# Kernel tuning notes

Hardware: AMD Instinct MI355X
Metric: run time of the kernel (lower is better)

The kernel has to match this reference:

```python
import jax, jax.numpy as jnp
import numpy as np

N = 200000      # nodes (Elliptic-scale transaction graph)
E = 400000      # directed edges
F_IN = 165      # node features
HID = 128
OUT = 2


def setup_inputs() -> dict:
    key = jax.random.key(0)
    k = jax.random.split(key, 5)
    x = jax.random.normal(k[0], (N, F_IN), dtype=jnp.float32)
    edge_index = jax.random.randint(k[1], (2, E), 0, N, dtype=jnp.int32)
    # GCNConv params (PyG: Linear without bias semantics differ slightly by
    # version; here weight + bias, bias added after aggregation)
    W1 = jax.random.normal(k[2], (F_IN, HID), dtype=jnp.float32) * (1.0 / np.sqrt(F_IN))
    b1 = jnp.zeros((HID,), dtype=jnp.float32)
    W2 = jax.random.normal(k[3], (HID, OUT), dtype=jnp.float32) * (1.0 / np.sqrt(HID))
    b2 = jnp.zeros((OUT,), dtype=jnp.float32)
    return {"x": x, "edge_index": edge_index, "W1": W1, "b1": b1, "W2": W2, "b2": b2}


def _gcn_conv(h, edge_index, W, b):
    """PyG GCNConv: out = D^{-1/2} (A + I) D^{-1/2} (h @ W) + b."""
    h = h @ W                                    # [N, F_out]
    loop = jnp.arange(N, dtype=edge_index.dtype)
    src = jnp.concatenate([edge_index[0], loop])  # add self-loops
    dst = jnp.concatenate([edge_index[1], loop])
    # degree over destination nodes (self-loops guarantee deg >= 1)
    deg = jax.ops.segment_sum(jnp.ones_like(dst, dtype=h.dtype), dst, num_segments=N)
    dinv = jax.lax.rsqrt(deg)
    norm = dinv[src] * dinv[dst]                 # [E+N]
    msgs = h[src] * norm[:, None]                # gather + scale
    out = jax.ops.segment_sum(msgs, dst, num_segments=N)  # scatter-add
    return out + b


def reference(x, edge_index, W1, b1, W2, b2):
    h = _gcn_conv(x, edge_index, W1, b1)
    # torch.relu then F.dropout(training=False) (identity) then torch.relu:
    # in eval mode relu(relu(h)) == relu(h)
    h = jnp.maximum(h, 0.0)
    return _gcn_conv(h, edge_index, W2, b2)
```

## Files before the change

kernel.cpp:

```cpp
#include <hip/hip_runtime.h>
#include <hip/hip_bf16.h>

typedef __attribute__((ext_vector_type(8))) short bf16x8;
typedef __attribute__((ext_vector_type(4))) float f32x4;

#define N_NODES 200000
#define N_EDGES 400000
#define F_IN    165
#define HID     128
#define BM      32
#define N_TILES 6250
#define KSTEPS  6
#define CAP     32

__device__ __forceinline__ uint bf16r(float f) {
  uint u = __float_as_uint(f);
  return (u + 0x7FFFu + ((u >> 16) & 1u)) >> 16;
}

__device__ __forceinline__ uint pkbf(float a, float b) {
  uint r;
  asm("v_cvt_pk_bf16_f32 %0, %1, %2" : "=v"(r) : "v"(a), "v"(b));
  return r;
}

__device__ __forceinline__ void gload16(const void* gp, void* lp) {
  __builtin_amdgcn_global_load_lds(
      (const __attribute__((address_space(1))) unsigned int*)gp,
      (__attribute__((address_space(3))) unsigned int*)lp, 16, 0, 0);
}


__global__ __launch_bounds__(256) void k_init(const float* __restrict__ W1,
                                              ushort* __restrict__ Wf,
                                              uint4* __restrict__ cursor) {
  int b = blockIdx.x;
  int tid = threadIdx.x;
  if (b < 96) {
    int id = b * 256 + tid;
    int j = id & 7;
    int lane = (id >> 3) & 63;
    int rem = id >> 9;
    int s = rem % 6;
    int ct = rem / 6;
    int k = s * 32 + (lane >> 4) * 8 + j;
    int col = ct * 16 + (lane & 15);
    float v = (k < F_IN) ? W1[k * HID + col] : 0.f;
    Wf[id] = (ushort)bf16r(v);
  } else {
    int i = (b - 96) * 256 + tid;
    if (i < 50000) cursor[i] = make_uint4(0, 0, 0, 0);
  }
}


__global__ __launch_bounds__(256) void k_gemm1p(const float* __restrict__ x,
                                                const ushort* __restrict__ Wf,
                                                const int* __restrict__ ei,
                                                int* __restrict__ cursor,
                                                int* __restrict__ slots,
                                                uint* __restrict__ g) {
  __shared__ float xs[BM * F_IN];
  const int tid  = threadIdx.x;
  const int wave = tid >> 6;
  const int lane = tid & 63;
  const int r15  = lane & 15;
  const int kg   = lane >> 4;

  if (tid < 64) {
    int e = blockIdx.x * 64 + tid;
    int d = ei[N_EDGES + e];
    int pos = atomicAdd(&cursor[d], 1);
    if (pos < CAP) slots[d * CAP + pos] = ei[e];
  }

  bf16x8 bfrag[2][KSTEPS];
  #pragma unroll
  for (int t = 0; t < 2; ++t) {
    int ct = wave * 2 + t;
    #pragma unroll
    for (int s = 0; s < KSTEPS; ++s)
      bfrag[t][s] = *(const bf16x8*)(Wf + (size_t)(((ct * KSTEPS + s) * 64 + lane) << 3));
  }

  const size_t tb = (size_t)blockIdx.x * (BM * F_IN);
  #pragma unroll
  for (int it = 0; it < 5; ++it) {
    gload16(x + tb + (size_t)(it * 256 + tid) * 4,
            (char*)xs + (size_t)(it * 256 + wave * 64) * 16);
  }
  if (tid < 40) {
    int c = 1280 + tid;
    *(float4*)((char*)xs + (size_t)c * 16) = *(const float4*)(x + tb + (size_t)c * 4);
  }
  __syncthreads();

  f32x4 acc[2][2];
  #pragma unroll
  for (int rg = 0; rg < 2; ++rg) {
    acc[rg][0] = (f32x4){0.f, 0.f, 0.f, 0.f};
    acc[rg][1] = (f32x4){0.f, 0.f, 0.f, 0.f};
  }

  #pragma unroll
  for (int rg = 0; rg < 2; ++rg) {
    const float* rp0 = xs + (rg * 16 + r15) * F_IN;
    #pragma unroll
    for (int s = 0; s < KSTEPS; ++s) {
      uint o0, o1, o2, o3;
      if (s < 5) {
        const float* rp = rp0 + s * 32 + kg * 8;
        o0 = pkbf(rp[0], rp[1]);
        o1 = pkbf(rp[2], rp[3]);
        o2 = pkbf(rp[4], rp[5]);
        o3 = pkbf(rp[6], rp[7]);
      } else {
        o0 = o1 = o2 = o3 = 0u;
        if (kg == 0) {
          const float* rp = rp0 + 160;
          o0 = pkbf(rp[0], rp[1]);
          o1 = pkbf(rp[2], rp[3]);
          o2 = pkbf(rp[4], 0.f);
        }
      }
      uint4 uu = make_uint4(o0, o1, o2, o3);
      bf16x8 a = *(bf16x8*)&uu;
      acc[rg][0] = __builtin_amdgcn_mfma_f32_16x16x32_bf16(a, bfrag[0][s], acc[rg][0], 0, 0, 0);
      acc[rg][1] = __builtin_amdgcn_mfma_f32_16x16x32_bf16(a, bfrag[1][s], acc[rg][1], 0, 0, 0);
    }
  }

  int base = blockIdx.x * BM;
  #pragma unroll
  for (int rg = 0; rg < 2; ++rg) {
    #pragma unroll
    for (int r = 0; r < 4; ++r) {
      int row = base + rg * 16 + kg * 4 + r;
      uint u = pkbf(acc[rg][0][r], acc[rg][1][r]);
      g[(size_t)row * 64 + wave * 16 + r15] = u;
    }
  }
}


__global__ __launch_bounds__(256) void k_agg1(const uint* __restrict__ g,
                                              const int* __restrict__ cursor,
                                              const int* __restrict__ slots,
                                              const float* __restrict__ b1,
                                              const float* __restrict__ W2,
                                              float* __restrict__ g2) {
  const int tid  = threadIdx.x;
  const int lane = tid & 63;
  const int wave = tid >> 6;
  const int sub  = lane >> 4;
  const int fl   = lane & 15;

  float  b1lo[4], b1hi[4];
  float2 w2lo[4], w2hi[4];
  #pragma unroll
  for (int k = 0; k < 4; ++k) {
    int dw = fl * 4 + k;
    int c0 = ((dw >> 4) << 5) + (dw & 15);
    b1lo[k] = b1[c0];
    b1hi[k] = b1[c0 + 16];
    w2lo[k] = *(const float2*)&W2[c0 * 2];
    w2hi[k] = *(const float2*)&W2[(c0 + 16) * 2];
  }

  int degs[8], slotv[8];
  #pragma unroll
  for (int it = 0; it < 8; ++it) {
    int node = blockIdx.x * 128 + it * 16 + wave * 4 + sub;
    int cn = min(node, N_NODES - 1);
    degs[it]  = cursor[cn];
    slotv[it] = slots[cn * CAP + fl];
  }

  #pragma unroll
  for (int it = 0; it < 8; ++it) {
    int node = blockIdx.x * 128 + it * 16 + wave * 4 + sub;
    if (node < N_NODES) {
      int deg = degs[it];
      float dv = rsqrtf(1.0f + (float)deg);
      int dcap = min(deg, 16);
      int srcl = (fl < dcap) ? slotv[it] : node;

      uint4 v = *(const uint4*)&g[(size_t)node * 64 + fl * 4];
      float sx0 = dv * __uint_as_float(v.x << 16), sy0 = dv * __uint_as_float(v.x & 0xFFFF0000u);
      float sx1 = dv * __uint_as_float(v.y << 16), sy1 = dv * __uint_as_float(v.y & 0xFFFF0000u);
      float sx2 = dv * __uint_as_float(v.z << 16), sy2 = dv * __uint_as_float(v.z & 0xFFFF0000u);
      float sx3 = dv * __uint_as_float(v.w << 16), sy3 = dv * __uint_as_float(v.w & 0xFFFF0000u);

      #pragma unroll
      for (int j = 0; j < 4; ++j) {
        int s = __shfl(srcl, sub * 16 + j);
        float wj = (j < dcap) ? rsqrtf(1.0f + (float)cursor[s]) : 0.f;
        uint4 w = *(const uint4*)&g[(size_t)s * 64 + fl * 4];
        sx0 = fmaf(__uint_as_float(w.x << 16), wj, sx0);
        sy0 = fmaf(__uint_as_float(w.x & 0xFFFF0000u), wj, sy0);
        sx1 = fmaf(__uint_as_float(w.y << 16), wj, sx1);
        sy1 = fmaf(__uint_as_float(w.y & 0xFFFF0000u), wj, sy1);
        sx2 = fmaf(__uint_as_float(w.z << 16), wj, sx2);
        sy2 = fmaf(__uint_as_float(w.z & 0xFFFF0000u), wj, sy2);
        sx3 = fmaf(__uint_as_float(w.w << 16), wj, sx3);
        sy3 = fmaf(__uint_as_float(w.w & 0xFFFF0000u), wj, sy3);
      }
      for (int j = 4; j < dcap; ++j) {
        int s = __shfl(srcl, sub * 16 + j);
        float wj = rsqrtf(1.0f + (float)cursor[s]);
        uint4 w = *(const uint4*)&g[(size_t)s * 64 + fl * 4];
        sx0 = fmaf(__uint_as_float(w.x << 16), wj, sx0);
        sy0 = fmaf(__uint_as_float(w.x & 0xFFFF0000u), wj, sy0);
        sx1 = fmaf(__uint_as_float(w.y << 16), wj, sx1);
        sy1 = fmaf(__uint_as_float(w.y & 0xFFFF0000u), wj, sy1);
        sx2 = fmaf(__uint_as_float(w.z << 16), wj, sx2);
        sy2 = fmaf(__uint_as_float(w.z & 0xFFFF0000u), wj, sy2);
        sx3 = fmaf(__uint_as_float(w.w << 16), wj, sx3);
        sy3 = fmaf(__uint_as_float(w.w & 0xFFFF0000u), wj, sy3);
      }
      for (int e = 16; e < min(deg, CAP); ++e) {
        int s = slots[node * CAP + e];
        float wj = rsqrtf(1.0f + (float)cursor[s]);
        uint4 w = *(const uint4*)&g[(size_t)s * 64 + fl * 4];
        sx0 = fmaf(__uint_as_float(w.x << 16), wj, sx0);
        sy0 = fmaf(__uint_as_float(w.x & 0xFFFF0000u), wj, sy0);
        sx1 = fmaf(__uint_as_float(w.y << 16), wj, sx1);
        sy1 = fmaf(__uint_as_float(w.y & 0xFFFF0000u), wj, sy1);
        sx2 = fmaf(__uint_as_float(w.z << 16), wj, sx2);
        sy2 = fmaf(__uint_as_float(w.z & 0xFFFF0000u), wj, sy2);
        sx3 = fmaf(__uint_as_float(w.w << 16), wj, sx3);
        sy3 = fmaf(__uint_as_float(w.w & 0xFFFF0000u), wj, sy3);
      }

      float h, p0 = 0.f, p1 = 0.f;
      h = fmaxf(fmaf(sx0, dv, b1lo[0]), 0.f); p0 = fmaf(h, w2lo[0].x, p0); p1 = fmaf(h, w2lo[0].y, p1);
      h = fmaxf(fmaf(sy0, dv, b1hi[0]), 0.f); p0 = fmaf(h, w2hi[0].x, p0); p1 = fmaf(h, w2hi[0].y, p1);
      h = fmaxf(fmaf(sx1, dv, b1lo[1]), 0.f); p0 = fmaf(h, w2lo[1].x, p0); p1 = fmaf(h, w2lo[1].y, p1);
      h = fmaxf(fmaf(sy1, dv, b1hi[1]), 0.f); p0 = fmaf(h, w2hi[1].x, p0); p1 = fmaf(h, w2hi[1].y, p1);
      h = fmaxf(fmaf(sx2, dv, b1lo[2]), 0.f); p0 = fmaf(h, w2lo[2].x, p0); p1 = fmaf(h, w2lo[2].y, p1);
      h = fmaxf(fmaf(sy2, dv, b1hi[2]), 0.f); p0 = fmaf(h, w2hi[2].x, p0); p1 = fmaf(h, w2hi[2].y, p1);
      h = fmaxf(fmaf(sx3, dv, b1lo[3]), 0.f); p0 = fmaf(h, w2lo[3].x, p0); p1 = fmaf(h, w2lo[3].y, p1);
      h = fmaxf(fmaf(sy3, dv, b1hi[3]), 0.f); p0 = fmaf(h, w2hi[3].x, p0); p1 = fmaf(h, w2hi[3].y, p1);

      #pragma unroll
      for (int off = 1; off < 16; off <<= 1) {
        p0 += __shfl_xor(p0, off);
        p1 += __shfl_xor(p1, off);
      }
      if (fl == 0) {
        *(float2*)&g2[(size_t)node * 2] = make_float2(p0 * dv, p1 * dv);
      }
    }
  }
}


__global__ __launch_bounds__(256) void k_agg2(const float2* __restrict__ g2,
                                              const int* __restrict__ cursor,
                                              const int* __restrict__ slots,
                                              const float* __restrict__ b2,
                                              float* __restrict__ out) {
  int i = blockIdx.x * 256 + threadIdx.x;
  if (i >= N_NODES) return;
  float2 s = g2[i];
  int deg = cursor[i];
  int dcap = min(deg, CAP);
  for (int e = 0; e < dcap; ++e) {
    float2 m = g2[slots[i * CAP + e]];
    s.x += m.x;
    s.y += m.y;
  }
  float dv = rsqrtf(1.0f + (float)deg);
  float2 o;
  o.x = fmaf(s.x, dv, b2[0]);
  o.y = fmaf(s.y, dv, b2[1]);
  *(float2*)&out[(size_t)i * 2] = o;
}


extern "C" void kernel_launch(void* const* d_in, const int* in_sizes, int n_in,
                              void* d_out, int out_size, void* d_ws, size_t ws_size,
                              hipStream_t stream) {
  const float* x  = (const float*)d_in[0];
  const int*   ei = (const int*)d_in[1];
  const float* W1 = (const float*)d_in[2];
  const float* b1 = (const float*)d_in[3];
  const float* W2 = (const float*)d_in[4];
  const float* b2 = (const float*)d_in[5];
  float* out = (float*)d_out;

  char* ws = (char*)d_ws;
  size_t off = 0;
  auto take = [&](size_t bytes) -> char* {
    char* p = ws + off;
    off = (off + bytes + 255) & ~(size_t)255;
    return p;
  };
  int*    cursor = (int*)   take((size_t)N_NODES * 4);
  int*    slots  = (int*)   take((size_t)N_NODES * CAP * 4);
  float*  g2     = (float*) take((size_t)N_NODES * 2 * 4);
  ushort* Wf     = (ushort*)take((size_t)8 * KSTEPS * 64 * 8 * 2);
  uint*   g      = (uint*)  take((size_t)N_NODES * 64 * 4);
  (void)ws_size; (void)in_sizes; (void)n_in; (void)out_size;

  k_init<<<292, 256, 0, stream>>>(W1, Wf, (uint4*)cursor);
  k_gemm1p<<<N_TILES, 256, 0, stream>>>(x, Wf, ei, cursor, slots, g);
  k_agg1<<<1563, 256, 0, stream>>>(g, cursor, slots, b1, W2, g2);
  k_agg2<<<(N_NODES + 255) / 256, 256, 0, stream>>>((const float2*)g2, cursor,
                                                    slots, b2, out);
}
```

Measured before the change: 100.1 us.

## Repartition gemm1 tile so each wave owns 16 rows and all columns

The GEMM kernel now uses 128 threads (2 waves) per 32-row tile. Each wave computes 16 rows across all 8 column tiles, instead of 4 waves each covering 32 rows and 2 column tiles. The A fragment (fp32 to bf16 conversion from LDS) is built once per wave rather than twice, which cuts redundant LDS reads and conversions. W fragments are loaded from global/L2 inside the k-loop instead of being preloaded into registers. The trade-off is more weight loads per wave and fewer waves per block for latency hiding; the edge-slot fill in the first 64 threads is unchanged.

```diff
diff --git a/kernel.cpp b/kernel.cpp
--- a/kernel.cpp
+++ b/kernel.cpp
@@ -54,7 +54,7 @@
 }
 
 
-__global__ __launch_bounds__(256) void k_gemm1p(const float* __restrict__ x,
+__global__ __launch_bounds__(128) void k_gemm1p(const float* __restrict__ x,
                                                 const ushort* __restrict__ Wf,
                                                 const int* __restrict__ ei,
                                                 int* __restrict__ cursor,
@@ -74,20 +74,11 @@
     if (pos < CAP) slots[d * CAP + pos] = ei[e];
   }
 
-  bf16x8 bfrag[2][KSTEPS];
-  #pragma unroll
-  for (int t = 0; t < 2; ++t) {
-    int ct = wave * 2 + t;
-    #pragma unroll
-    for (int s = 0; s < KSTEPS; ++s)
-      bfrag[t][s] = *(const bf16x8*)(Wf + (size_t)(((ct * KSTEPS + s) * 64 + lane) << 3));
-  }
-
   const size_t tb = (size_t)blockIdx.x * (BM * F_IN);
   #pragma unroll
-  for (int it = 0; it < 5; ++it) {
-    gload16(x + tb + (size_t)(it * 256 + tid) * 4,
-            (char*)xs + (size_t)(it * 256 + wave * 64) * 16);
+  for (int it = 0; it < 10; ++it) {
+    gload16(x + tb + (size_t)(it * 128 + tid) * 4,
+            (char*)xs + (size_t)(it * 128 + wave * 64) * 16);
   }
   if (tid < 40) {
     int c = 1280 + tid;
@@ -95,49 +86,46 @@
   }
   __syncthreads();
 
-  f32x4 acc[2][2];
-  #pragma unroll
-  for (int rg = 0; rg < 2; ++rg) {
-    acc[rg][0] = (f32x4){0.f, 0.f, 0.f, 0.f};
-    acc[rg][1] = (f32x4){0.f, 0.f, 0.f, 0.f};
-  }
-
-  #pragma unroll
-  for (int rg = 0; rg < 2; ++rg) {
-    const float* rp0 = xs + (rg * 16 + r15) * F_IN;
-    #pragma unroll
-    for (int s = 0; s < KSTEPS; ++s) {
-      uint o0, o1, o2, o3;
-      if (s < 5) {
-        const float* rp = rp0 + s * 32 + kg * 8;
+  f32x4 acc[8];
+  #pragma unroll
+  for (int ct = 0; ct < 8; ++ct) acc[ct] = (f32x4){0.f, 0.f, 0.f, 0.f};
+
+  const float* rp0 = xs + (wave * 16 + r15) * F_IN;
+  #pragma unroll
+  for (int s = 0; s < KSTEPS; ++s) {
+    uint o0, o1, o2, o3;
+    if (s < 5) {
+      const float* rp = rp0 + s * 32 + kg * 8;
+      o0 = pkbf(rp[0], rp[1]);
+      o1 = pkbf(rp[2], rp[3]);
+      o2 = pkbf(rp[4], rp[5]);
+      o3 = pkbf(rp[6], rp[7]);
+    } else {
+      o0 = o1 = o2 = o3 = 0u;
+      if (kg == 0) {
+        const float* rp = rp0 + 160;
         o0 = pkbf(rp[0], rp[1]);
         o1 = pkbf(rp[2], rp[3]);
-        o2 = pkbf(rp[4], rp[5]);
-        o3 = pkbf(rp[6], rp[7]);
-      } else {
-        o0 = o1 = o2 = o3 = 0u;
-        if (kg == 0) {
-          const float* rp = rp0 + 160;
-          o0 = pkbf(rp[0], rp[1]);
-          o1 = pkbf(rp[2], rp[3]);
-          o2 = pkbf(rp[4], 0.f);
-        }
-      }
-      uint4 uu = make_uint4(o0, o1, o2, o3);
-      bf16x8 a = *(bf16x8*)&uu;
-      acc[rg][0] = __builtin_amdgcn_mfma_f32_16x16x32_bf16(a, bfrag[0][s], acc[rg][0], 0, 0, 0);
-      acc[rg][1] = __builtin_amdgcn_mfma_f32_16x16x32_bf16(a, bfrag[1][s], acc[rg][1], 0, 0, 0);
+        o2 = pkbf(rp[4], 0.f);
+      }
+    }
+    uint4 uu = make_uint4(o0, o1, o2, o3);
+    bf16x8 a = *(bf16x8*)&uu;
+    #pragma unroll
+    for (int ct = 0; ct < 8; ++ct) {
+      bf16x8 b = *(const bf16x8*)(Wf + (size_t)(((ct * KSTEPS + s) * 64 + lane) << 3));
+      acc[ct] = __builtin_amdgcn_mfma_f32_16x16x32_bf16(a, b, acc[ct], 0, 0, 0);
     }
   }
 
   int base = blockIdx.x * BM;
   #pragma unroll
-  for (int rg = 0; rg < 2; ++rg) {
+  for (int r = 0; r < 4; ++r) {
+    int row = base + wave * 16 + kg * 4 + r;
     #pragma unroll
-    for (int r = 0; r < 4; ++r) {
-      int row = base + rg * 16 + kg * 4 + r;
-      uint u = pkbf(acc[rg][0][r], acc[rg][1][r]);
-      g[(size_t)row * 64 + wave * 16 + r15] = u;
+    for (int cp = 0; cp < 4; ++cp) {
+      uint u = pkbf(acc[2 * cp][r], acc[2 * cp + 1][r]);
+      g[(size_t)row * 64 + cp * 16 + r15] = u;
     }
   }
 }
@@ -304,7 +292,7 @@
   (void)ws_size; (void)in_sizes; (void)n_in; (void)out_size;
 
   k_init<<<292, 256, 0, stream>>>(W1, Wf, (uint4*)cursor);
-  k_gemm1p<<<N_TILES, 256, 0, stream>>>(x, Wf, ei, cursor, slots, g);
+  k_gemm1p<<<N_TILES, 128, 0, stream>>>(x, Wf, ei, cursor, slots, g);
   k_agg1<<<1563, 256, 0, stream>>>(g, cursor, slots, b1, W2, g2);
   k_agg2<<<(N_NODES + 255) / 256, 256, 0, stream>>>((const float2*)g2, cursor,
                                                     slots, b2, out);
```

Result: slower. 111.7 us (+11.5%).
